# Kernel tuning notes

Hardware: AMD Instinct MI355X
Metric: run time of the kernel (lower is better)

## Reference

```python
import jax, jax.numpy as jnp
import numpy as np

MSE_WEIGHT = 0.7
CORR_WEIGHT = 0.3
EPS = 1e-8
B, L = 256, 65536


def setup_inputs() -> dict:
    key = jax.random.key(0)
    k1, k2 = jax.random.split(key)
    y_pred = jax.random.normal(k1, (B, L), dtype=jnp.float32)
    y_true = jax.random.normal(k2, (B, L), dtype=jnp.float32)
    return {"y_pred": y_pred, "y_true": y_true}


def reference(y_pred, y_true):
    # MSE over all elements (nn.MSELoss default 'mean')
    mse_loss = jnp.mean((y_pred - y_true) ** 2)

    # Vectorized per-sample Pearson correlation (original loops over batch)
    xm = y_true - jnp.mean(y_true, axis=1, keepdims=True)   # [B, L]
    ym = y_pred - jnp.mean(y_pred, axis=1, keepdims=True)   # [B, L]
    r_num = jnp.sum(xm * ym, axis=1)                        # [B]
    r_den = jnp.sqrt(jnp.sum(xm * xm, axis=1) * jnp.sum(ym * ym, axis=1))
    r_den = jnp.maximum(r_den, EPS)
    r = r_num / r_den                                       # [B]
    corr_loss = jnp.mean(1.0 - r)

    total_loss = MSE_WEIGHT * mse_loss + CORR_WEIGHT * corr_loss
    return total_loss.reshape(1)  # original returns shape-[1] tensor
```

## Files before the change

### kernel.cpp

```cpp
#include <hip/hip_runtime.h>

#define B_ROWS   256
#define L_COLS   65536
#define SLICES   8
#define THREADS  256
#define NBLOCKS  (B_ROWS * SLICES)
#define V_ROW    (L_COLS / 4)
#define V_SLICE  (V_ROW / SLICES)

#define GLOAD(dst, ptr) \
    asm volatile("global_load_dwordx4 %0, %1, off" : "=v"(dst) : "v"(ptr) : "memory")

#define WAITV(n) do { \
    asm volatile("s_waitcnt vmcnt(" #n ")" ::: "memory"); \
    __builtin_amdgcn_sched_barrier(0); } while (0)

__global__ __launch_bounds__(THREADS, 4)
void signal_loss_partials(const float4* __restrict__ pred,
                          const float4* __restrict__ trgt,
                          float* __restrict__ ws)
{
    const int bid   = blockIdx.x;
    const int row   = bid >> 3;
    const int slice = bid & (SLICES - 1);
    const size_t base = (size_t)row * V_ROW + (size_t)slice * V_SLICE + threadIdx.x;
    const float4* P = pred + base;
    const float4* T = trgt + base;

    float4 a0, a1, at0, at1;
    float4 b0, b1, bt0, bt1;
    float4 c0, c1, ct0, ct1;
    float4 d0, d1, dt0, dt1;

    GLOAD(a0,  P + 0 * THREADS); GLOAD(a1,  P + 1 * THREADS);
    GLOAD(at0, T + 0 * THREADS); GLOAD(at1, T + 1 * THREADS);
    GLOAD(b0,  P + 2 * THREADS); GLOAD(b1,  P + 3 * THREADS);
    GLOAD(bt0, T + 2 * THREADS); GLOAD(bt1, T + 3 * THREADS);
    GLOAD(c0,  P + 4 * THREADS); GLOAD(c1,  P + 5 * THREADS);
    GLOAD(ct0, T + 4 * THREADS); GLOAD(ct1, T + 5 * THREADS);
    GLOAD(d0,  P + 6 * THREADS); GLOAD(d1,  P + 7 * THREADS);
    GLOAD(dt0, T + 6 * THREADS); GLOAD(dt1, T + 7 * THREADS);

    float sp = 0.f, st = 0.f, spp = 0.f, stt = 0.f, spt = 0.f;

#define ACC1(p, t) do { \
    sp  += (p).x + (p).y + (p).z + (p).w; \
    st  += (t).x + (t).y + (t).z + (t).w; \
    spp += (p).x*(p).x + (p).y*(p).y + (p).z*(p).z + (p).w*(p).w; \
    stt += (t).x*(t).x + (t).y*(t).y + (t).z*(t).z + (t).w*(t).w; \
    spt += (p).x*(t).x + (p).y*(t).y + (p).z*(t).z + (p).w*(t).w; } while (0)

    WAITV(12); ACC1(a0, at0); ACC1(a1, at1);
    WAITV(8);  ACC1(b0, bt0); ACC1(b1, bt1);
    WAITV(4);  ACC1(c0, ct0); ACC1(c1, ct1);
    WAITV(0);  ACC1(d0, dt0); ACC1(d1, dt1);

#undef ACC1

    #pragma unroll
    for (int off = 32; off >= 1; off >>= 1) {
        sp  += __shfl_down(sp,  off);
        st  += __shfl_down(st,  off);
        spp += __shfl_down(spp, off);
        stt += __shfl_down(stt, off);
        spt += __shfl_down(spt, off);
    }

    __shared__ float red[4][5];
    const int lane = threadIdx.x & 63;
    const int wave = threadIdx.x >> 6;
    if (lane == 0) {
        red[wave][0] = sp;  red[wave][1] = st;  red[wave][2] = spp;
        red[wave][3] = stt; red[wave][4] = spt;
    }
    __syncthreads();
    if (threadIdx.x == 0) {
        float* dst = ws + (size_t)bid * 8;
        #pragma unroll
        for (int k = 0; k < 5; ++k)
            dst[k] = red[0][k] + red[1][k] + red[2][k] + red[3][k];
        dst[5] = 0.f; dst[6] = 0.f; dst[7] = 0.f;
    }
}

__global__ __launch_bounds__(B_ROWS)
void signal_loss_finalize(const float4* __restrict__ ws4,
                          float* __restrict__ out)
{
    const int row = threadIdx.x;

    float4 lo[SLICES], hi[SLICES];
    #pragma unroll
    for (int sl = 0; sl < SLICES; ++sl) {
        const size_t rec = ((size_t)row * SLICES + sl) * 2;
        lo[sl] = ws4[rec + 0];
        hi[sl] = ws4[rec + 1];
    }

    double s0=0.0, s1=0.0, s2=0.0, s3=0.0, s4=0.0;
    #pragma unroll
    for (int sl = 0; sl < SLICES; ++sl) {
        s0 += (double)lo[sl].x;
        s1 += (double)lo[sl].y;
        s2 += (double)lo[sl].z;
        s3 += (double)lo[sl].w;
        s4 += (double)hi[sl].x;
    }

    const double n = (double)L_COLS;
    const double num   = s4 - s0 * s1 / n;
    const double den_t = s3 - s1 * s1 / n;
    const double den_p = s2 - s0 * s0 / n;
    double den = sqrt(den_t * den_p);
    den = den > 1e-8 ? den : 1e-8;
    double romr = 1.0 - num / den;
    double sd   = s2 + s3 - 2.0 * s4;

    #pragma unroll
    for (int off = 32; off >= 1; off >>= 1) {
        romr += __shfl_down(romr, off);
        sd   += __shfl_down(sd,   off);
    }
    __shared__ double w0[4], w1[4];
    const int lane = threadIdx.x & 63;
    const int wave = threadIdx.x >> 6;
    if (lane == 0) { w0[wave] = romr; w1[wave] = sd; }
    __syncthreads();
    if (threadIdx.x == 0) {
        const double corr = (w0[0] + w0[1] + w0[2] + w0[3]) / (double)B_ROWS;
        const double mse  = (w1[0] + w1[1] + w1[2] + w1[3])
                          / ((double)B_ROWS * (double)L_COLS);
        out[0] = (float)(0.7 * mse + 0.3 * corr);
    }
}

extern "C" void kernel_launch(void* const* d_in, const int* in_sizes, int n_in,
                              void* d_out, int out_size, void* d_ws, size_t ws_size,
                              hipStream_t stream) {
    const float4* pred = (const float4*)d_in[0];
    const float4* trgt = (const float4*)d_in[1];
    float* ws  = (float*)d_ws;
    float* out = (float*)d_out;

    signal_loss_partials<<<NBLOCKS, THREADS, 0, stream>>>(pred, trgt, ws);
    signal_loss_finalize<<<1, B_ROWS, 0, stream>>>((const float4*)ws, out);
}
```

Before: 28.84 us.

## Fuse finalize into partials kernel via last-block atomic counter

Merges the two kernels into one: each block writes its partial sums with cache-bypassing stores, then increments a global atomic counter, and the last block to arrive performs the final per-row Pearson and MSE reduction. The per-block records are split into a packed 4-float array and a separate float array to shrink finalize reads. This removes the second kernel launch and its launch gap, but adds a memset launch for the counter plus an atomic and a store-drain wait in every block.

After: 44.99 us. 56.0% more time.

```diff
diff --git a/kernel.cpp b/kernel.cpp
--- a/kernel.cpp
+++ b/kernel.cpp
@@ -8,29 +8,44 @@
 #define V_ROW    (L_COLS / 4)
 #define V_SLICE  (V_ROW / SLICES)
 
+typedef float v4f __attribute__((ext_vector_type(4)));
+
+#define WS_RECA_OFF   64
+#define WS_RECB_OFF   (64 + NBLOCKS * 16)
+
 #define GLOAD(dst, ptr) \
     asm volatile("global_load_dwordx4 %0, %1, off" : "=v"(dst) : "v"(ptr) : "memory")
-
+#define GLOAD_SC(dst, ptr) \
+    asm volatile("global_load_dwordx4 %0, %1, off sc0 sc1" : "=v"(dst) : "v"(ptr) : "memory")
+#define GSTORE4_SC(ptr, val) \
+    asm volatile("global_store_dwordx4 %0, %1, off sc0 sc1" :: "v"(ptr), "v"(val) : "memory")
+#define GSTORE1_SC(ptr, val) \
+    asm volatile("global_store_dword %0, %1, off sc0 sc1" :: "v"(ptr), "v"(val) : "memory")
 #define WAITV(n) do { \
     asm volatile("s_waitcnt vmcnt(" #n ")" ::: "memory"); \
     __builtin_amdgcn_sched_barrier(0); } while (0)
 
 __global__ __launch_bounds__(THREADS, 4)
-void signal_loss_partials(const float4* __restrict__ pred,
-                          const float4* __restrict__ trgt,
-                          float* __restrict__ ws)
+void signal_loss_fused(const v4f* __restrict__ pred,
+                       const v4f* __restrict__ trgt,
+                       char* __restrict__ ws,
+                       float* __restrict__ out)
 {
     const int bid   = blockIdx.x;
     const int row   = bid >> 3;
     const int slice = bid & (SLICES - 1);
     const size_t base = (size_t)row * V_ROW + (size_t)slice * V_SLICE + threadIdx.x;
-    const float4* P = pred + base;
-    const float4* T = trgt + base;
+    const v4f* P = pred + base;
+    const v4f* T = trgt + base;
 
-    float4 a0, a1, at0, at1;
-    float4 b0, b1, bt0, bt1;
-    float4 c0, c1, ct0, ct1;
-    float4 d0, d1, dt0, dt1;
+    unsigned int* counter = (unsigned int*)ws;
+    v4f*   recA = (v4f*)(ws + WS_RECA_OFF);
+    float* recB = (float*)(ws + WS_RECB_OFF);
+
+    v4f a0, a1, at0, at1;
+    v4f b0, b1, bt0, bt1;
+    v4f c0, c1, ct0, ct1;
+    v4f d0, d1, dt0, dt1;
 
     GLOAD(a0,  P + 0 * THREADS); GLOAD(a1,  P + 1 * THREADS);
     GLOAD(at0, T + 0 * THREADS); GLOAD(at1, T + 1 * THREADS);
@@ -54,7 +69,6 @@
     WAITV(8);  ACC1(b0, bt0); ACC1(b1, bt1);
     WAITV(4);  ACC1(c0, ct0); ACC1(c1, ct1);
     WAITV(0);  ACC1(d0, dt0); ACC1(d1, dt1);
-
 #undef ACC1
 
     #pragma unroll
@@ -67,6 +81,7 @@
     }
 
     __shared__ float red[4][5];
+    __shared__ unsigned int lastflag;
     const int lane = threadIdx.x & 63;
     const int wave = threadIdx.x >> 6;
     if (lane == 0) {
@@ -75,73 +90,81 @@
     }
     __syncthreads();
     if (threadIdx.x == 0) {
-        float* dst = ws + (size_t)bid * 8;
+        v4f rec;
+        rec.x = red[0][0] + red[1][0] + red[2][0] + red[3][0];
+        rec.y = red[0][1] + red[1][1] + red[2][1] + red[3][1];
+        rec.z = red[0][2] + red[1][2] + red[2][2] + red[3][2];
+        rec.w = red[0][3] + red[1][3] + red[2][3] + red[3][3];
+        const float sptv = red[0][4] + red[1][4] + red[2][4] + red[3][4];
+        v4f*   dstA = recA + bid;
+        float* dstB = recB + bid;
+        GSTORE4_SC(dstA, rec);
+        GSTORE1_SC(dstB, sptv);
+        asm volatile("s_waitcnt vmcnt(0)" ::: "memory");
+        const unsigned int old = __hip_atomic_fetch_add(
+            counter, 1u, __ATOMIC_RELAXED, __HIP_MEMORY_SCOPE_AGENT);
+        lastflag = (old == (unsigned int)(NBLOCKS - 1)) ? 1u : 0u;
+    }
+    __syncthreads();
+    if (!lastflag) return;
+
+    {
+        const int r = threadIdx.x;
+        const v4f* rpA = recA + (size_t)r * SLICES;
+        const v4f* rpB = (const v4f*)(recB + (size_t)r * SLICES);
+        v4f l0,l1,l2,l3,l4,l5,l6,l7;
+        v4f q0,q1;
+        GLOAD_SC(l0, rpA + 0); GLOAD_SC(l1, rpA + 1);
+        GLOAD_SC(l2, rpA + 2); GLOAD_SC(l3, rpA + 3);
+        GLOAD_SC(l4, rpA + 4); GLOAD_SC(l5, rpA + 5);
+        GLOAD_SC(l6, rpA + 6); GLOAD_SC(l7, rpA + 7);
+        GLOAD_SC(q0, rpB + 0); GLOAD_SC(q1, rpB + 1);
+        WAITV(0);
+
+        double s0=0.0, s1=0.0, s2=0.0, s3=0.0, s4=0.0;
+#define ACCF(l) do { \
+        s0 += (double)(l).x; s1 += (double)(l).y; \
+        s2 += (double)(l).z; s3 += (double)(l).w; } while (0)
+        ACCF(l0); ACCF(l1); ACCF(l2); ACCF(l3);
+        ACCF(l4); ACCF(l5); ACCF(l6); ACCF(l7);
+#undef ACCF
+        s4 = (double)q0.x + (double)q0.y + (double)q0.z + (double)q0.w
+           + (double)q1.x + (double)q1.y + (double)q1.z + (double)q1.w;
+
+        const double n = (double)L_COLS;
+        const double num   = s4 - s0 * s1 / n;
+        const double den_t = s3 - s1 * s1 / n;
+        const double den_p = s2 - s0 * s0 / n;
+        double den = sqrt(den_t * den_p);
+        den = den > 1e-8 ? den : 1e-8;
+        double romr = 1.0 - num / den;
+        double sd   = s2 + s3 - 2.0 * s4;
+
         #pragma unroll
-        for (int k = 0; k < 5; ++k)
-            dst[k] = red[0][k] + red[1][k] + red[2][k] + red[3][k];
-        dst[5] = 0.f; dst[6] = 0.f; dst[7] = 0.f;
-    }
-}
-
-__global__ __launch_bounds__(B_ROWS)
-void signal_loss_finalize(const float4* __restrict__ ws4,
-                          float* __restrict__ out)
-{
-    const int row = threadIdx.x;
-
-    float4 lo[SLICES], hi[SLICES];
-    #pragma unroll
-    for (int sl = 0; sl < SLICES; ++sl) {
-        const size_t rec = ((size_t)row * SLICES + sl) * 2;
-        lo[sl] = ws4[rec + 0];
-        hi[sl] = ws4[rec + 1];
-    }
-
-    double s0=0.0, s1=0.0, s2=0.0, s3=0.0, s4=0.0;
-    #pragma unroll
-    for (int sl = 0; sl < SLICES; ++sl) {
-        s0 += (double)lo[sl].x;
-        s1 += (double)lo[sl].y;
-        s2 += (double)lo[sl].z;
-        s3 += (double)lo[sl].w;
-        s4 += (double)hi[sl].x;
-    }
-
-    const double n = (double)L_COLS;
-    const double num   = s4 - s0 * s1 / n;
-    const double den_t = s3 - s1 * s1 / n;
-    const double den_p = s2 - s0 * s0 / n;
-    double den = sqrt(den_t * den_p);
-    den = den > 1e-8 ? den : 1e-8;
-    double romr = 1.0 - num / den;
-    double sd   = s2 + s3 - 2.0 * s4;
-
-    #pragma unroll
-    for (int off = 32; off >= 1; off >>= 1) {
-        romr += __shfl_down(romr, off);
-        sd   += __shfl_down(sd,   off);
-    }
-    __shared__ double w0[4], w1[4];
-    const int lane = threadIdx.x & 63;
-    const int wave = threadIdx.x >> 6;
-    if (lane == 0) { w0[wave] = romr; w1[wave] = sd; }
-    __syncthreads();
-    if (threadIdx.x == 0) {
-        const double corr = (w0[0] + w0[1] + w0[2] + w0[3]) / (double)B_ROWS;
-        const double mse  = (w1[0] + w1[1] + w1[2] + w1[3])
-                          / ((double)B_ROWS * (double)L_COLS);
-        out[0] = (float)(0.7 * mse + 0.3 * corr);
+        for (int off = 32; off >= 1; off >>= 1) {
+            romr += __shfl_down(romr, off);
+            sd   += __shfl_down(sd,   off);
+        }
+        __shared__ double w0[4], w1[4];
+        if (lane == 0) { w0[wave] = romr; w1[wave] = sd; }
+        __syncthreads();
+        if (threadIdx.x == 0) {
+            const double corr = (w0[0] + w0[1] + w0[2] + w0[3]) / (double)B_ROWS;
+            const double mse  = (w1[0] + w1[1] + w1[2] + w1[3])
+                              / ((double)B_ROWS * (double)L_COLS);
+            out[0] = (float)(0.7 * mse + 0.3 * corr);
+        }
     }
 }
 
 extern "C" void kernel_launch(void* const* d_in, const int* in_sizes, int n_in,
                               void* d_out, int out_size, void* d_ws, size_t ws_size,
                               hipStream_t stream) {
-    const float4* pred = (const float4*)d_in[0];
-    const float4* trgt = (const float4*)d_in[1];
-    float* ws  = (float*)d_ws;
+    const v4f* pred = (const v4f*)d_in[0];
+    const v4f* trgt = (const v4f*)d_in[1];
+    char* ws   = (char*)d_ws;
     float* out = (float*)d_out;
 
-    signal_loss_partials<<<NBLOCKS, THREADS, 0, stream>>>(pred, trgt, ws);
-    signal_loss_finalize<<<1, B_ROWS, 0, stream>>>((const float4*)ws, out);
+    (void)hipMemsetAsync(ws, 0, sizeof(unsigned int), stream);
+    signal_loss_fused<<<NBLOCKS, THREADS, 0, stream>>>(pred, trgt, ws, out);
 }
```
